# Kernel tuning notes

Hardware: AMD Instinct MI355X
Metric: run time of the kernel (lower is better)

Reference implementation:

```python
import jax, jax.numpy as jnp
import numpy as np

N = 50000        # nodes (spots)
E = 1_600_000    # edges per graph (avg degree 32)
NFEAT = 512
NHID1 = 256
NHID2 = 64
ATT_H = 16       # SpatialAttention hidden_size default
BN_EPS = 1e-5


def setup_inputs() -> dict:
    key = jax.random.key(0)
    ks = iter(jax.random.split(key, 40))
    rn = lambda shape, s=0.05: jax.random.normal(next(ks), shape, jnp.float32) * s
    inp = {
        'x': jax.random.normal(next(ks), (N, NFEAT), jnp.float32),
        'sadj_edges': jax.random.randint(next(ks), (2, E), 0, N, jnp.int32),
        'fadj_edges': jax.random.randint(next(ks), (2, E), 0, N, jnp.int32),
        # GIN gc1 MLP: nfeat->nhid1->nhid1
        'Wg1a': rn((NFEAT, NHID1)), 'bg1a': jnp.zeros((NHID1,), jnp.float32),
        'Wg1b': rn((NHID1, NHID1)), 'bg1b': jnp.zeros((NHID1,), jnp.float32),
        # GIN gc2 MLP: nhid1->nhid2->nhid2
        'Wg2a': rn((NHID1, NHID2)), 'bg2a': jnp.zeros((NHID2,), jnp.float32),
        'Wg2b': rn((NHID2, NHID2)), 'bg2b': jnp.zeros((NHID2,), jnp.float32),
        # SpatialAttention: Linear(nhid2->16), Tanh, Linear(16->1, no bias)
        'Wa1': rn((NHID2, ATT_H)), 'ba1': jnp.zeros((ATT_H,), jnp.float32),
        'Wa2': rn((ATT_H, 1)),
        # MLP: nhid2->nhid2
        'Wmlp': rn((NHID2, NHID2)), 'bmlp': jnp.zeros((NHID2,), jnp.float32),
        # decoder: Linear(nhid2->nhid1) + BN(eval) + ReLU
        'Wd': rn((NHID2, NHID1)), 'bd': jnp.zeros((NHID1,), jnp.float32),
        'bn_gamma': jnp.ones((NHID1,), jnp.float32),
        'bn_beta': jnp.zeros((NHID1,), jnp.float32),
        'bn_mean': jnp.zeros((NHID1,), jnp.float32),
        'bn_var': jnp.ones((NHID1,), jnp.float32),
        # heads: nhid1->nfeat
        'Wpi': rn((NHID1, NFEAT)), 'bpi': jnp.zeros((NFEAT,), jnp.float32),
        'Wv': rn((NHID1, NFEAT)), 'bv': jnp.zeros((NFEAT,), jnp.float32),
        'Wmu': rn((NHID1, NFEAT)), 'bmu': jnp.zeros((NFEAT,), jnp.float32),
    }
    return inp


def _gin_conv(x, src, dst, W1, b1, W2, b2):
    # GINConv with eps=0: mlp(x + sum_{j in N(i)} x_j)
    agg = jax.ops.segment_sum(x[src], dst, num_segments=N)
    h = x + agg
    h = jax.nn.relu(h @ W1 + b1) @ W2 + b2
    return h


def _gin(x, edges, Wg1a, bg1a, Wg1b, bg1b, Wg2a, bg2a, Wg2b, bg2b):
    src, dst = edges[0], edges[1]
    h = jax.nn.relu(_gin_conv(x, src, dst, Wg1a, bg1a, Wg1b, bg1b))
    # dropout p=0 / eval -> identity
    h = _gin_conv(h, src, dst, Wg2a, bg2a, Wg2b, bg2b)
    return h


def reference(x, sadj_edges, fadj_edges,
              Wg1a, bg1a, Wg1b, bg1b, Wg2a, bg2a, Wg2b, bg2b,
              Wa1, ba1, Wa2, Wmlp, bmlp,
              Wd, bd, bn_gamma, bn_beta, bn_mean, bn_var,
              Wpi, bpi, Wv, bv, Wmu, bmu):
    emb1 = _gin(x, sadj_edges, Wg1a, bg1a, Wg1b, bg1b, Wg2a, bg2a, Wg2b, bg2b)
    emb2 = _gin(x, fadj_edges, Wg1a, bg1a, Wg1b, bg1b, Wg2a, bg2a, Wg2b, bg2b)
    # com = (MGIN(x,sadj)+MGIN(x,fadj))/2 == (emb1+emb2)/2 in eval mode
    com = (emb1 + emb2) * 0.5
    z = jnp.stack([emb1, com, emb2], axis=1)              # [N, 3, nhid2]
    # SpatialAttention
    w = jnp.tanh(z @ Wa1 + ba1) @ Wa2                     # [N, 3, 1]
    beta = jax.nn.softmax(w, axis=1)
    emb = (beta * z).sum(axis=1)                          # [N, nhid2]
    emb = emb @ Wmlp + bmlp
    # decoder (BatchNorm in eval mode: running stats)
    h = emb @ Wd + bd
    h = (h - bn_mean) * jax.lax.rsqrt(bn_var + BN_EPS) * bn_gamma + bn_beta
    h = jax.nn.relu(h)
    pi = jax.nn.sigmoid(h @ Wpi + bpi)
    var = jnp.clip(jax.nn.softplus(h @ Wv + bv), 1e-4, 1e4)
    mean = jnp.clip(jnp.exp(h @ Wmu + bmu), 1e-5, 1e6)
    return (emb1, emb2, emb, pi, var, mean)
```

## Files before the change

kernel.cpp:

```cpp
#include <hip/hip_runtime.h>
#include <hip/hip_bf16.h>
#include <cstdint>
#include <cstddef>

#define NFEAT 512
#define NHID1 256
#define NHID2 64
#define ATTH  16

typedef __attribute__((ext_vector_type(8))) short short8v;
typedef __attribute__((ext_vector_type(8))) unsigned short ushort8v;
typedef __attribute__((ext_vector_type(4))) float f32x4;

enum { EPI_NONE=0, EPI_RELU=1, EPI_BNRELU=2, EPI_HEADS3=3 };

static __device__ __forceinline__ float bf2f(unsigned short u) {
    return __uint_as_float(((unsigned int)u) << 16);
}
static __device__ __forceinline__ unsigned short f2bf(float f) {
    __hip_bfloat16 h = __float2bfloat16(f);
    return *reinterpret_cast<unsigned short*>(&h);
}

__global__ __launch_bounds__(256) void convert_x_kernel(const float* __restrict__ in,
                                                        unsigned short* __restrict__ out, long n4) {
    long i = blockIdx.x * (long)blockDim.x + threadIdx.x;
    long stride = (long)gridDim.x * blockDim.x;
    for (; i < n4; i += stride) {
        float4 v = reinterpret_cast<const float4*>(in)[i];
        ushort4 o;
        o.x = f2bf(v.x); o.y = f2bf(v.y); o.z = f2bf(v.z); o.w = f2bf(v.w);
        reinterpret_cast<ushort4*>(out)[i] = o;
    }
}

struct WSpec { const float* W; unsigned short* Wt; int K, Nn; };
struct WPack { WSpec s[8]; };

__global__ __launch_bounds__(256) void convert_wt_all_kernel(WPack p) {
    WSpec sp = p.s[blockIdx.y];
    int total = sp.K * sp.Nn;
    for (int idx = blockIdx.x * 256 + threadIdx.x; idx < total; idx += gridDim.x * 256) {
        int n = idx / sp.K, k = idx % sp.K;
        sp.Wt[idx] = f2bf(sp.W[(size_t)k * sp.Nn + n]);
    }
}

template<int EPI, int OUT_BF16>
__global__ __launch_bounds__(256) void mfma_gemm_kernel(
    const unsigned short* __restrict__ A, const unsigned short* __restrict__ Bt,
    const float* __restrict__ bias, void* __restrict__ Cout,
    int M, int K, int Nn, long headStride,
    const float* __restrict__ bp0, const float* __restrict__ bp1,
    const float* __restrict__ bp2, const float* __restrict__ bp3)
{
    __shared__ unsigned short As[128 * 32];
    __shared__ unsigned short Bs[128 * 32];
    const int t = threadIdx.x;
    const int w = t >> 6, l = t & 63;
    const int wr = w >> 1, wc = w & 1;
    const int rowBase = blockIdx.y * 128, colBase = blockIdx.x * 128;

    f32x4 acc[4][4];
    #pragma unroll
    for (int m = 0; m < 4; ++m)
        #pragma unroll
        for (int n = 0; n < 4; ++n) acc[m][n] = (f32x4){0.f, 0.f, 0.f, 0.f};

    const int c0 = w * 2, c1 = w * 2 + 1;
    const int r0 = c0 * 16 + (l >> 2), r1 = c1 * 16 + (l >> 2);
    const int kid = (l & 3) * 8;
    int ar0 = rowBase + r0; if (ar0 >= M) ar0 = M - 1;
    int ar1 = rowBase + r1; if (ar1 >= M) ar1 = M - 1;
    int br0 = colBase + r0; if (br0 >= Nn) br0 = Nn - 1;
    int br1 = colBase + r1; if (br1 >= Nn) br1 = Nn - 1;
    const unsigned short* a0p = A + (size_t)ar0 * K + kid;
    const unsigned short* a1p = A + (size_t)ar1 * K + kid;
    const unsigned short* b0p = Bt + (size_t)br0 * K + kid;
    const unsigned short* b1p = Bt + (size_t)br1 * K + kid;

    const int frow = (l & 15), fk = (l >> 4) * 8;

    for (int k0 = 0; k0 < K; k0 += 32) {
        __builtin_amdgcn_global_load_lds(
            (const __attribute__((address_space(1))) void*)(a0p + k0),
            (__attribute__((address_space(3))) void*)(As + c0 * 512), 16, 0, 0);
        __builtin_amdgcn_global_load_lds(
            (const __attribute__((address_space(1))) void*)(a1p + k0),
            (__attribute__((address_space(3))) void*)(As + c1 * 512), 16, 0, 0);
        __builtin_amdgcn_global_load_lds(
            (const __attribute__((address_space(1))) void*)(b0p + k0),
            (__attribute__((address_space(3))) void*)(Bs + c0 * 512), 16, 0, 0);
        __builtin_amdgcn_global_load_lds(
            (const __attribute__((address_space(1))) void*)(b1p + k0),
            (__attribute__((address_space(3))) void*)(Bs + c1 * 512), 16, 0, 0);
        __syncthreads();

        short8v a[4], b[4];
        #pragma unroll
        for (int m = 0; m < 4; ++m)
            a[m] = *reinterpret_cast<const short8v*>(As + (wr * 64 + m * 16 + frow) * 32 + fk);
        #pragma unroll
        for (int n = 0; n < 4; ++n)
            b[n] = *reinterpret_cast<const short8v*>(Bs + (wc * 64 + n * 16 + frow) * 32 + fk);
        #pragma unroll
        for (int m = 0; m < 4; ++m)
            #pragma unroll
            for (int n = 0; n < 4; ++n)
                acc[m][n] = __builtin_amdgcn_mfma_f32_16x16x32_bf16(a[m], b[n], acc[m][n], 0, 0, 0);
        __syncthreads();
    }

    #pragma unroll
    for (int n = 0; n < 4; ++n) {
        int c = colBase + wc * 64 + n * 16 + (l & 15);
        if (c >= Nn) continue;
        float bia = 0.f, g = 0.f, bb = 0.f, mm = 0.f, iv = 0.f;
        int hh = 0, cc = c;
        if (EPI == EPI_HEADS3) {
            hh = c >> 9; cc = c & 511;
            bia = (hh == 0) ? bp0[cc] : (hh == 1) ? bp1[cc] : bp2[cc];
        } else {
            if (bias) bia = bias[c];
            if (EPI == EPI_BNRELU) {
                g = bp0[c]; bb = bp1[c]; mm = bp2[c];
                iv = rsqrtf(bp3[c] + 1e-5f);
            }
        }
        #pragma unroll
        for (int m = 0; m < 4; ++m) {
            #pragma unroll
            for (int j = 0; j < 4; ++j) {
                int r = rowBase + wr * 64 + m * 16 + (l >> 4) * 4 + j;
                if (r >= M) continue;
                float v = acc[m][n][j] + bia;
                if (EPI == EPI_RELU) {
                    v = fmaxf(v, 0.f);
                } else if (EPI == EPI_BNRELU) {
                    v = (v - mm) * iv * g + bb;
                    v = fmaxf(v, 0.f);
                } else if (EPI == EPI_HEADS3) {
                    if (hh == 0) {
                        v = 1.f / (1.f + expf(-v));
                    } else if (hh == 1) {
                        float sp = (v > 20.f) ? v : log1pf(expf(v));
                        v = fminf(fmaxf(sp, 1e-4f), 1e4f);
                    } else {
                        v = fminf(fmaxf(expf(v), 1e-5f), 1e6f);
                    }
                }
                if (EPI == EPI_HEADS3)
                    ((float*)Cout)[(size_t)hh * headStride + (size_t)r * 512 + cc] = v;
                else if (OUT_BF16)
                    ((unsigned short*)Cout)[(size_t)r * Nn + c] = f2bf(v);
                else
                    ((float*)Cout)[(size_t)r * Nn + c] = v;
            }
        }
    }
}

__global__ void hist2_kernel(const int* __restrict__ edst0, const int* __restrict__ edst1,
                             int* __restrict__ deg, int e, int nHalf) {
    int i = blockIdx.x * blockDim.x + threadIdx.x;
    if (i < 2 * e) {
        int d = (i < e) ? edst0[i] : (edst1[i - e] + nHalf);
        atomicAdd(&deg[d], 1);
    }
}

__global__ __launch_bounds__(1024) void scan_block_kernel(const int* __restrict__ deg,
                                                          int* __restrict__ excl,
                                                          int* __restrict__ bsum, int n) {
    __shared__ int buf[1024];
    int i = blockIdx.x * 1024 + (int)threadIdx.x;
    int v = (i < n) ? deg[i] : 0;
    buf[threadIdx.x] = v;
    __syncthreads();
    for (int off = 1; off < 1024; off <<= 1) {
        int tv = (threadIdx.x >= (unsigned)off) ? buf[threadIdx.x - off] : 0;
        __syncthreads();
        buf[threadIdx.x] += tv;
        __syncthreads();
    }
    if (i < n) excl[i] = buf[threadIdx.x] - v;
    if (threadIdx.x == 1023) bsum[blockIdx.x] = buf[1023];
}

__global__ __launch_bounds__(1024) void scan_tops_kernel(int* __restrict__ bsum, int nb) {
    __shared__ int buf[1024];
    int v = ((int)threadIdx.x < nb) ? bsum[threadIdx.x] : 0;
    buf[threadIdx.x] = v;
    __syncthreads();
    for (int off = 1; off < 1024; off <<= 1) {
        int tv = (threadIdx.x >= (unsigned)off) ? buf[threadIdx.x - off] : 0;
        __syncthreads();
        buf[threadIdx.x] += tv;
        __syncthreads();
    }
    if ((int)threadIdx.x < nb) bsum[threadIdx.x] = buf[threadIdx.x] - v;
}

__global__ void scan_add_kernel(int* __restrict__ row_start, const int* __restrict__ bsum,
                                const int* __restrict__ deg, int* __restrict__ cursor, int n) {
    int i = blockIdx.x * blockDim.x + threadIdx.x;
    if (i < n) {
        int s = row_start[i] + bsum[i >> 10];
        row_start[i] = s;
        cursor[i] = s;
        if (i == n - 1) row_start[n] = s + deg[i];
    }
}

#define SC_EPT 8
__global__ __launch_bounds__(256) void scatter_win_kernel(
    const int* __restrict__ sadj, const int* __restrict__ fadj,
    int* __restrict__ cursor, int* __restrict__ csr_src,
    int e, int nHalf, int winSize)
{
    const int win = blockIdx.x & 7;
    const int chunk = blockIdx.x >> 3;
    const int lo = win * winSize, hi = lo + winSize;
    const int base = chunk * (256 * SC_EPT);
    const int e2 = 2 * e;
    #pragma unroll
    for (int r = 0; r < SC_EPT; ++r) {
        int i = base + r * 256 + (int)threadIdx.x;
        if (i >= e2) break;
        int src, d;
        if (i < e) { src = sadj[i];     d = sadj[e + i]; }
        else       { int j = i - e; src = fadj[j]; d = fadj[e + j] + nHalf; }
        if (d >= lo && d < hi) {
            int pos = atomicAdd(&cursor[d], 1);
            csr_src[pos] = src;
        }
    }
}

template<int F, bool SRC_OFFSET>
__global__ __launch_bounds__(256) void agg_combine_kernel(
    const unsigned short* __restrict__ xin, const int* __restrict__ row_start,
    const int* __restrict__ csr_src, const float* __restrict__ bias,
    unsigned short* __restrict__ out, int n2, int nHalf)
{
    constexpr int LPN = F / 8;
    int node = blockIdx.x * (256 / LPN) + (int)threadIdx.x / LPN;
    int lane = (int)threadIdx.x % LPN;
    if (node >= n2) return;
    const int srcAdd  = (SRC_OFFSET && node >= nHalf) ? nHalf : 0;
    const int selfIdx = SRC_OFFSET ? node : (node >= nHalf ? node - nHalf : node);
    int beg = row_start[node], end = row_start[node + 1];
    float a[8];
    #pragma unroll
    for (int j = 0; j < 8; ++j) a[j] = 0.f;
    int e = beg;
    for (; e + 4 <= end; e += 4) {
        int s0 = csr_src[e] + srcAdd, s1 = csr_src[e+1] + srcAdd;
        int s2 = csr_src[e+2] + srcAdd, s3 = csr_src[e+3] + srcAdd;
        ushort8v v0 = *reinterpret_cast<const ushort8v*>(xin + (size_t)s0 * F + lane * 8);
        ushort8v v1 = *reinterpret_cast<const ushort8v*>(xin + (size_t)s1 * F + lane * 8);
        ushort8v v2 = *reinterpret_cast<const ushort8v*>(xin + (size_t)s2 * F + lane * 8);
        ushort8v v3 = *reinterpret_cast<const ushort8v*>(xin + (size_t)s3 * F + lane * 8);
        #pragma unroll
        for (int j = 0; j < 8; ++j)
            a[j] += bf2f(v0[j]) + bf2f(v1[j]) + bf2f(v2[j]) + bf2f(v3[j]);
    }
    for (; e < end; ++e) {
        int s = csr_src[e] + srcAdd;
        ushort8v v = *reinterpret_cast<const ushort8v*>(xin + (size_t)s * F + lane * 8);
        #pragma unroll
        for (int j = 0; j < 8; ++j) a[j] += bf2f(v[j]);
    }
    ushort8v sv = *reinterpret_cast<const ushort8v*>(xin + (size_t)selfIdx * F + lane * 8);
    ushort8v o;
    #pragma unroll
    for (int j = 0; j < 8; ++j)
        o[j] = f2bf(fmaxf(bf2f(sv[j]) + a[j] + bias[lane * 8 + j], 0.f));
    *reinterpret_cast<ushort8v*>(out + (size_t)node * F + lane * 8) = o;
}

__global__ __launch_bounds__(256) void attn_mlp_kernel(
    const float* __restrict__ emb1, const float* __restrict__ emb2,
    const float* __restrict__ Wa1, const float* __restrict__ ba1,
    const float* __restrict__ Wa2, const float* __restrict__ Wmlp,
    const float* __restrict__ bmlp, float* __restrict__ out,
    unsigned short* __restrict__ out_bf, int n)
{
    __shared__ float sWa1[NHID2][ATTH];
    __shared__ float sba1[ATTH], sWa2[ATTH];
    __shared__ float sWmlp[NHID2][NHID2 + 1];
    __shared__ float sbmlp[NHID2];
    __shared__ float zs[4][3][NHID2 + 1];
    __shared__ float part[4][3][ATTH];
    __shared__ float sbeta[4][3];
    __shared__ float es[4][NHID2 + 1];

    int t = threadIdx.x;
    for (int idx = t; idx < NHID2 * ATTH; idx += 256) sWa1[idx / ATTH][idx % ATTH] = Wa1[idx];
    if (t < ATTH) { sba1[t] = ba1[t]; sWa2[t] = Wa2[t]; }
    for (int idx = t; idx < NHID2 * NHID2; idx += 256) sWmlp[idx / NHID2][idx % NHID2] = Wmlp[idx];
    if (t < NHID2) sbmlp[t] = bmlp[t];

    int w = t >> 6, lane = t & 63;

    for (int rep = 0; rep < 4; ++rep) {
        int node = blockIdx.x * 16 + rep * 4 + w;
        float z0 = 0.f, z2 = 0.f;
        if (node < n) {
            z0 = emb1[(size_t)node * NHID2 + lane];
            z2 = emb2[(size_t)node * NHID2 + lane];
        }
        zs[w][0][lane] = z0;
        zs[w][1][lane] = 0.5f * (z0 + z2);
        zs[w][2][lane] = z2;
        __syncthreads();

        if (t < 192) {
            int ww = t / 48, k = (t / 16) % 3, h = t % 16;
            float p = 0.f;
            #pragma unroll 8
            for (int i = 0; i < NHID2; ++i) p += zs[ww][k][i] * sWa1[i][h];
            part[ww][k][h] = tanhf(p + sba1[h]) * sWa2[h];
        }
        __syncthreads();
        if (t < 12) {
            int ww = t / 3, k = t % 3;
            float s = 0.f;
            #pragma unroll
            for (int h = 0; h < ATTH; ++h) s += part[ww][k][h];
            part[ww][k][0] = s;
        }
        __syncthreads();
        if (t < 4) {
            float w0 = part[t][0][0], w1 = part[t][1][0], w2 = part[t][2][0];
            float m = fmaxf(w0, fmaxf(w1, w2));
            float e0 = expf(w0 - m), e1 = expf(w1 - m), e2 = expf(w2 - m);
            float d = e0 + e1 + e2;
            sbeta[t][0] = e0 / d; sbeta[t][1] = e1 / d; sbeta[t][2] = e2 / d;
        }
        __syncthreads();
        es[w][lane] = sbeta[w][0] * zs[w][0][lane] + sbeta[w][1] * zs[w][1][lane]
                    + sbeta[w][2] * zs[w][2][lane];
        __syncthreads();
        if (node < n) {
            float v = sbmlp[lane];
            #pragma unroll 8
            for (int i = 0; i < NHID2; ++i) v = fmaf(es[w][i], sWmlp[i][lane], v);
            out[(size_t)node * NHID2 + lane] = v;
            out_bf[(size_t)node * NHID2 + lane] = f2bf(v);
        }
        __syncthreads();
    }
}

extern "C" void kernel_launch(void* const* d_in, const int* in_sizes, int n_in,
                              void* d_out, int out_size, void* d_ws, size_t ws_size,
                              hipStream_t stream) {
    const float* x    = (const float*)d_in[0];
    const int*   sadj = (const int*)d_in[1];
    const int*   fadj = (const int*)d_in[2];
    const int N = in_sizes[0] / NFEAT;
    const int E = in_sizes[1] / 2;
    const int N2 = 2 * N;
    const float* Wg1a = (const float*)d_in[3];
    const float* bg1a = (const float*)d_in[4];
    const float* Wg1b = (const float*)d_in[5];
    const float* bg1b = (const float*)d_in[6];
    const float* Wg2a = (const float*)d_in[7];
    const float* bg2a = (const float*)d_in[8];
    const float* Wg2b = (const float*)d_in[9];
    const float* bg2b = (const float*)d_in[10];
    const float* Wa1  = (const float*)d_in[11];
    const float* ba1  = (const float*)d_in[12];
    const float* Wa2  = (const float*)d_in[13];
    const float* Wmlp = (const float*)d_in[14];
    const float* bmlp = (const float*)d_in[15];
    const float* Wd   = (const float*)d_in[16];
    const float* bd   = (const float*)d_in[17];
    const float* bn_g = (const float*)d_in[18];
    const float* bn_b = (const float*)d_in[19];
    const float* bn_m = (const float*)d_in[20];
    const float* bn_v = (const float*)d_in[21];
    const float* Wpi  = (const float*)d_in[22];
    const float* bpi  = (const float*)d_in[23];
    const float* Wv   = (const float*)d_in[24];
    const float* bv   = (const float*)d_in[25];
    const float* Wmu  = (const float*)d_in[26];
    const float* bmu  = (const float*)d_in[27];

    float* out   = (float*)d_out;
    float* emb1  = out;
    float* embO  = out + 2 * (size_t)N * NHID2;
    float* pi    = out + 3 * (size_t)N * NHID2;
    float* var_  = pi + (size_t)N * NFEAT;
    float* mean_ = var_ + (size_t)N * NFEAT;

    char* wsb = (char*)d_ws;
    auto alloc = [&](size_t bytes) { char* p = wsb; wsb += (bytes + 255) & ~(size_t)255; return p; };
    unsigned short* xw_bf   = (unsigned short*)alloc((size_t)N  * NHID1 * 2);
    unsigned short* hw_bf   = (unsigned short*)alloc((size_t)N2 * NHID2 * 2);
    unsigned short* h3_bf   = (unsigned short*)alloc((size_t)N2 * NHID2 * 2);
    unsigned short* embO_bf = (unsigned short*)alloc((size_t)N  * NHID2 * 2);
    unsigned short* hdec_bf = (unsigned short*)alloc((size_t)N  * NHID1 * 2);
    unsigned short* Wg1a_t  = (unsigned short*)alloc((size_t)NFEAT * NHID1 * 2);
    unsigned short* Wg1b_t  = (unsigned short*)alloc((size_t)NHID1 * NHID1 * 2);
    unsigned short* Wg2a_t  = (unsigned short*)alloc((size_t)NHID1 * NHID2 * 2);
    unsigned short* Wg2b_t  = (unsigned short*)alloc((size_t)NHID2 * NHID2 * 2);
    unsigned short* Wd_t    = (unsigned short*)alloc((size_t)NHID2 * NHID1 * 2);
    unsigned short* Wcat_t  = (unsigned short*)alloc((size_t)3 * NFEAT * NHID1 * 2);
    int* deg       = (int*)alloc((size_t)N2 * 4);
    int* row_start = (int*)alloc((size_t)(N2 + 1) * 4);
    int* cursor    = (int*)alloc((size_t)N2 * 4);
    int* bsum      = (int*)alloc((size_t)1024 * 4);
    int* csr_src   = (int*)alloc((size_t)2 * E * 4);

    unsigned short* x_bf  = (unsigned short*)mean_;
    unsigned short* h1_bf = (unsigned short*)pi;
    unsigned short* h_bf  = (unsigned short*)var_;

    const int gyN  = (N + 127) / 128;
    const int gyN2 = (N2 + 127) / 128;
    const int nb   = (N2 + 1023) / 1024;

    convert_x_kernel<<<2048, 256, 0, stream>>>(x, x_bf, (long)N * NFEAT / 4);
    WPack wp;
    wp.s[0] = {Wg1a, Wg1a_t, NFEAT, NHID1};
    wp.s[1] = {Wg1b, Wg1b_t, NHID1, NHID1};
    wp.s[2] = {Wg2a, Wg2a_t, NHID1, NHID2};
    wp.s[3] = {Wg2b, Wg2b_t, NHID2, NHID2};
    wp.s[4] = {Wd,   Wd_t,   NHID2, NHID1};
    wp.s[5] = {Wpi,  Wcat_t,                          NHID1, NFEAT};
    wp.s[6] = {Wv,   Wcat_t + (size_t)NFEAT * NHID1,  NHID1, NFEAT};
    wp.s[7] = {Wmu,  Wcat_t + (size_t)2 * NFEAT * NHID1, NHID1, NFEAT};
    convert_wt_all_kernel<<<dim3(64, 8), 256, 0, stream>>>(wp);

    hipMemsetAsync(deg, 0, (size_t)N2 * sizeof(int), stream);
    hist2_kernel<<<(2 * E + 255) / 256, 256, 0, stream>>>(sadj + E, fadj + E, deg, E, N);
    scan_block_kernel<<<nb, 1024, 0, stream>>>(deg, row_start, bsum, N2);
    scan_tops_kernel<<<1, 1024, 0, stream>>>(bsum, nb);
    scan_add_kernel<<<(N2 + 255) / 256, 256, 0, stream>>>(row_start, bsum, deg, cursor, N2);
    {
        const int chunks = (2 * E + 256 * SC_EPT - 1) / (256 * SC_EPT);
        const int winSize = (N2 + 7) / 8;
        scatter_win_kernel<<<chunks * 8, 256, 0, stream>>>(
            sadj, fadj, cursor, csr_src, E, N, winSize);
    }

    mfma_gemm_kernel<EPI_NONE,1><<<dim3(2, gyN), 256, 0, stream>>>(
        x_bf, Wg1a_t, nullptr, xw_bf, N, NFEAT, NHID1, 0,
        nullptr, nullptr, nullptr, nullptr);
    agg_combine_kernel<NHID1,false><<<(N2 * (NHID1/8) + 255) / 256, 256, 0, stream>>>(
        xw_bf, row_start, csr_src, bg1a, h1_bf, N2, N);
    mfma_gemm_kernel<EPI_RELU,1><<<dim3(2, gyN2), 256, 0, stream>>>(
        h1_bf, Wg1b_t, bg1b, h_bf, N2, NHID1, NHID1, 0,
        nullptr, nullptr, nullptr, nullptr);
    mfma_gemm_kernel<EPI_NONE,1><<<dim3(1, gyN2), 256, 0, stream>>>(
        h_bf, Wg2a_t, nullptr, hw_bf, N2, NHID1, NHID2, 0,
        nullptr, nullptr, nullptr, nullptr);
    agg_combine_kernel<NHID2,true><<<(N2 * (NHID2/8) + 255) / 256, 256, 0, stream>>>(
        hw_bf, row_start, csr_src, bg2a, h3_bf, N2, N);
    mfma_gemm_kernel<EPI_NONE,0><<<dim3(1, gyN2), 256, 0, stream>>>(
        h3_bf, Wg2b_t, bg2b, emb1, N2, NHID2, NHID2, 0,
        nullptr, nullptr, nullptr, nullptr);

    attn_mlp_kernel<<<(N + 15) / 16, 256, 0, stream>>>(
        emb1, emb1 + (size_t)N * NHID2, Wa1, ba1, Wa2, Wmlp, bmlp, embO, embO_bf, N);

    mfma_gemm_kernel<EPI_BNRELU,1><<<dim3(2, gyN), 256, 0, stream>>>(
        embO_bf, Wd_t, bd, hdec_bf, N, NHID2, NHID1, 0,
        bn_g, bn_b, bn_m, bn_v);

    mfma_gemm_kernel<EPI_HEADS3,0><<<dim3(12, gyN), 256, 0, stream>>>(
        hdec_bf, Wcat_t, nullptr, pi, N, NHID1, 3 * NFEAT, (long)N * NFEAT,
        bpi, bv, bmu, nullptr);
}
```

Measured before the change: 1.076 ms.

## Stage GEMM epilogue through LDS for coalesced vector stores; use fast exp/log

The GEMM epilogue now writes each 32x128 slice of results into shared memory, reusing the operand tile buffers, and then stores them to global memory as float4 or ushort4 rows, so the output writes are coalesced instead of scattered scalar stores. The heads epilogue also switches to __expf and __logf intrinsics. This adds two block barriers per m-iteration and some loss of accuracy in the transcendental functions. Vector stores assume Nn is a multiple of 4 and that the 128-column tile does not straddle a head boundary.

```diff
diff --git a/kernel.cpp b/kernel.cpp
--- a/kernel.cpp
+++ b/kernel.cpp
@@ -54,8 +54,11 @@
     const float* __restrict__ bp0, const float* __restrict__ bp1,
     const float* __restrict__ bp2, const float* __restrict__ bp3)
 {
-    __shared__ unsigned short As[128 * 32];
-    __shared__ unsigned short Bs[128 * 32];
+    __shared__ __align__(16) char smem[32 * 132 * 4];
+    unsigned short* As = (unsigned short*)smem;
+    unsigned short* Bs = As + 128 * 32;
+    float* Es = (float*)smem;
+
     const int t = threadIdx.x;
     const int w = t >> 6, l = t & 63;
     const int wr = w >> 1, wc = w & 1;
@@ -111,28 +114,31 @@
         __syncthreads();
     }
 
+    const int colLoc = wc * 64 + (l & 15);
+    const int lrBase = wr * 16 + (l >> 4) * 4;
+    const int hh = colBase >> 9;
+    const int ccBase = colBase & 511;
+
     #pragma unroll
-    for (int n = 0; n < 4; ++n) {
-        int c = colBase + wc * 64 + n * 16 + (l & 15);
-        if (c >= Nn) continue;
-        float bia = 0.f, g = 0.f, bb = 0.f, mm = 0.f, iv = 0.f;
-        int hh = 0, cc = c;
-        if (EPI == EPI_HEADS3) {
-            hh = c >> 9; cc = c & 511;
-            bia = (hh == 0) ? bp0[cc] : (hh == 1) ? bp1[cc] : bp2[cc];
-        } else {
-            if (bias) bia = bias[c];
-            if (EPI == EPI_BNRELU) {
-                g = bp0[c]; bb = bp1[c]; mm = bp2[c];
-                iv = rsqrtf(bp3[c] + 1e-5f);
+    for (int m = 0; m < 4; ++m) {
+        #pragma unroll
+        for (int n = 0; n < 4; ++n) {
+            const int cl = colLoc + n * 16;
+            const int c  = colBase + cl;
+            const int cs = (c < Nn) ? c : 0;
+            float bia = 0.f, g = 0.f, bb = 0.f, mm = 0.f, iv = 0.f;
+            if (EPI == EPI_HEADS3) {
+                int cc = c & 511;
+                bia = (hh == 0) ? bp0[cc] : (hh == 1) ? bp1[cc] : bp2[cc];
+            } else {
+                if (bias) bia = bias[cs];
+                if (EPI == EPI_BNRELU) {
+                    g = bp0[cs]; bb = bp1[cs]; mm = bp2[cs];
+                    iv = rsqrtf(bp3[cs] + 1e-5f);
+                }
             }
-        }
-        #pragma unroll
-        for (int m = 0; m < 4; ++m) {
             #pragma unroll
             for (int j = 0; j < 4; ++j) {
-                int r = rowBase + wr * 64 + m * 16 + (l >> 4) * 4 + j;
-                if (r >= M) continue;
                 float v = acc[m][n][j] + bia;
                 if (EPI == EPI_RELU) {
                     v = fmaxf(v, 0.f);
@@ -141,22 +147,39 @@
                     v = fmaxf(v, 0.f);
                 } else if (EPI == EPI_HEADS3) {
                     if (hh == 0) {
-                        v = 1.f / (1.f + expf(-v));
+                        v = 1.f / (1.f + __expf(-v));
                     } else if (hh == 1) {
-                        float sp = (v > 20.f) ? v : log1pf(expf(v));
+                        float sp = (v > 20.f) ? v : __logf(1.f + __expf(v));
                         v = fminf(fmaxf(sp, 1e-4f), 1e4f);
                     } else {
-                        v = fminf(fmaxf(expf(v), 1e-5f), 1e6f);
+                        v = fminf(fmaxf(__expf(v), 1e-5f), 1e6f);
                     }
                 }
-                if (EPI == EPI_HEADS3)
-                    ((float*)Cout)[(size_t)hh * headStride + (size_t)r * 512 + cc] = v;
-                else if (OUT_BF16)
-                    ((unsigned short*)Cout)[(size_t)r * Nn + c] = f2bf(v);
-                else
-                    ((float*)Cout)[(size_t)r * Nn + c] = v;
+                Es[(lrBase + j) * 132 + cl] = v;
             }
         }
+        __syncthreads();
+        #pragma unroll
+        for (int p = 0; p < 4; ++p) {
+            const int flat = p * 1024 + t * 4;
+            const int r = flat >> 7, c = flat & 127;
+            const int R = rowBase + m * 16 + (r < 16 ? r : 48 + r);
+            const int C = colBase + c;
+            if (R < M && C < Nn) {
+                float4 v4 = *reinterpret_cast<const float4*>(Es + r * 132 + c);
+                if (EPI == EPI_HEADS3) {
+                    *reinterpret_cast<float4*>(
+                        (float*)Cout + (size_t)hh * headStride + (size_t)R * 512 + (ccBase + c)) = v4;
+                } else if (OUT_BF16) {
+                    ushort4 o;
+                    o.x = f2bf(v4.x); o.y = f2bf(v4.y); o.z = f2bf(v4.z); o.w = f2bf(v4.w);
+                    *reinterpret_cast<ushort4*>((unsigned short*)Cout + (size_t)R * Nn + C) = o;
+                } else {
+                    *reinterpret_cast<float4*>((float*)Cout + (size_t)R * Nn + C) = v4;
+                }
+            }
+        }
+        __syncthreads();
     }
 }
 
```

After: 883.4 us. -17.9%, faster.
